# Performance work log

Measured on AMD Instinct MI355X. Metric: run time of the kernel, lower is better.

## Reference

```python
import jax, jax.numpy as jnp
import numpy as np

B = 4          # number of prefill sequences (uniform cu_seqlens)
S = 1024       # tokens per sequence; total_tokens = B*S
SCALE = 0.08838834764831845  # head_dim ** -0.5


def setup_inputs() -> dict:
    key = jax.random.key(0)
    k1, k2, k3 = jax.random.split(key, 3)
    N, H, Hk, D = B * S, 16, 4, 128
    q = jax.random.normal(k1, (N, H, D), dtype=jnp.float32)
    k = jax.random.normal(k2, (N, Hk, D), dtype=jnp.float32)
    v = jax.random.normal(k3, (N, Hk, D), dtype=jnp.float32)
    k_cache = jnp.zeros((N, Hk * D), dtype=jnp.float32)
    v_cache = jnp.zeros((N, Hk * D), dtype=jnp.float32)
    slot_mapping = jnp.arange(N, dtype=jnp.int32)
    return {"q": q, "k": k, "v": v, "k_cache": k_cache,
            "v_cache": v_cache, "slot_mapping": slot_mapping}


def _store_kvcache(k, v, k_cache, v_cache, slot_mapping):
    # scatter token KV into flat paged cache; slot == -1 means skip
    N = k.shape[0]
    valid = slot_mapping >= 0
    slot = jnp.where(valid, slot_mapping, 0)
    k_flat = k.reshape(N, -1)
    v_flat = v.reshape(N, -1)
    kc = k_cache.at[slot].set(jnp.where(valid[:, None], k_flat, k_cache[slot]))
    vc = v_cache.at[slot].set(jnp.where(valid[:, None], v_flat, v_cache[slot]))
    return kc, vc


def _varlen_causal_attn(q, k, v):
    # q: [N, H, D], k/v: [N, Hk, D] with N = B*S uniform sequences (GQA)
    N, H, D = q.shape
    Hk = k.shape[1]
    G = H // Hk
    qb = q.reshape(B, S, Hk, G, D)
    kb = k.reshape(B, S, Hk, D)
    vb = v.reshape(B, S, Hk, D)
    # scores: [B, Hk, G, Sq, Sk]
    scores = jnp.einsum("bqhgd,bkhd->bhgqk", qb, kb) * jnp.float32(SCALE)
    causal = jnp.tril(jnp.ones((S, S), dtype=bool))  # [Sq, Sk]
    scores = jnp.where(causal, scores, jnp.float32(-1e30))
    p = jax.nn.softmax(scores, axis=-1)
    o = jnp.einsum("bhgqk,bkhd->bqhgd", p, vb)
    return o.reshape(N, H, D)


def reference(q, k, v, k_cache, v_cache, slot_mapping):
    kc, vc = _store_kvcache(k, v, k_cache, v_cache, slot_mapping)
    o = _varlen_causal_attn(q, k, v)
    return o, kc, vc
```

## Files before the change

kernel.cpp:

```cpp
#include <hip/hip_runtime.h>

typedef short bf16x8 __attribute__((ext_vector_type(8)));
typedef short bf16x4 __attribute__((ext_vector_type(4)));
typedef float f32x4 __attribute__((ext_vector_type(4)));

#define NB 4
#define SS 1024
#define NH 16
#define NHK 4
#define DD 128
#define NT 16
#define QSCALE 0.08838834764831845f
#define LOG2E 1.4426950408889634f

__device__ __forceinline__ float exp2v(float x) { return __builtin_amdgcn_exp2f(x); }

__device__ __forceinline__ short f2bf(float f) {
  unsigned u = __builtin_bit_cast(unsigned, f);
  u += 0x7fffu + ((u >> 16) & 1u);
  return (short)(u >> 16);
}
__device__ __forceinline__ unsigned pk2(float lo, float hi) {
  return ((unsigned)(unsigned short)f2bf(hi) << 16) | (unsigned)(unsigned short)f2bf(lo);
}

typedef __attribute__((address_space(1))) const unsigned gu32;
typedef __attribute__((address_space(3))) unsigned lu32;
__device__ __forceinline__ void gload16(const void* g, void* l) {
  __builtin_amdgcn_global_load_lds((gu32*)g, (lu32*)l, 16, 0, 0);
}

#define DRAIN_DMA()                                    \
  do {                                                 \
    asm volatile("s_waitcnt vmcnt(0)" ::: "memory");   \
    __builtin_amdgcn_sched_barrier(0);                 \
  } while (0)

__global__ __launch_bounds__(256) void scatter_kv_kernel(
    const float* __restrict__ k, const float* __restrict__ v,
    const int* __restrict__ slot, float* __restrict__ ko, float* __restrict__ vo) {
  int gid = blockIdx.x * blockDim.x + threadIdx.x;
  int tok = gid >> 7;
  int j = gid & 127;
  int s = slot[tok];
  if (s < 0) return;
  ((float4*)(ko + (size_t)s * 512))[j] = ((const float4*)(k + (size_t)tok * 512))[j];
  ((float4*)(vo + (size_t)s * 512))[j] = ((const float4*)(v + (size_t)tok * 512))[j];
}

__global__ __launch_bounds__(256) void prep_kernel(
    const float* __restrict__ k, const float* __restrict__ v,
    const int* __restrict__ slot,
    short* __restrict__ kimg, short* __restrict__ vimg,
    float* __restrict__ ko, float* __restrict__ vo) {
  __shared__ float lvf[64 * 129];
  const int blk = blockIdx.x;
  const int t = blk & 15;
  const int hk = (blk >> 4) & 3;
  const int b = blk >> 6;
  const long tb = (long)b * SS + t * 64;
  const int tid = threadIdx.x;
  short* ki = kimg + (size_t)blk * 8192;
  short* vi = vimg + (size_t)blk * 8192;

#pragma unroll
  for (int p = 0; p < 4; ++p) {
    int c = p * 256 + tid;
    int byte0 = c * 16;
    int row = byte0 >> 8;
    int d0 = (byte0 & 255) >> 1;
    const float* src = k + ((tb + row) * NHK + hk) * DD + d0;
    float4 x = *(const float4*)src;
    float4 y = *(const float4*)(src + 4);
    uint4 pk = {pk2(x.x, x.y), pk2(x.z, x.w), pk2(y.x, y.y), pk2(y.z, y.w)};
    *(uint4*)((char*)ki + (byte0 ^ ((row & 7) << 4))) = pk;
    const float* vs = v + ((tb + row) * NHK + hk) * DD + d0;
    float4 vx = *(const float4*)vs;
    float4 vy = *(const float4*)(vs + 4);
    int sl = slot[tb + row];
    if (sl >= 0) {
      float* kd = ko + (size_t)sl * 512 + hk * 128 + d0;
      *(float4*)kd = x; *(float4*)(kd + 4) = y;
      float* vd = vo + (size_t)sl * 512 + hk * 128 + d0;
      *(float4*)vd = vx; *(float4*)(vd + 4) = vy;
    }
    float* dst = &lvf[row * 129 + d0];
    dst[0] = vx.x; dst[1] = vx.y; dst[2] = vx.z; dst[3] = vx.w;
    dst[4] = vy.x; dst[5] = vy.y; dst[6] = vy.z; dst[7] = vy.w;
  }
  __syncthreads();
#pragma unroll
  for (int p = 0; p < 4; ++p) {
    int c16 = p * 256 + tid;
    int d = c16 >> 3;
    int c8 = c16 & 7;
    int pos0 = c8 * 8;
    int cblk = pos0 >> 5;
    int lg = (pos0 >> 3) & 3;
    int kvb = cblk * 32 + lg * 4;
    float f[8];
#pragma unroll
    for (int j = 0; j < 4; ++j) f[j] = lvf[(kvb + j) * 129 + d];
#pragma unroll
    for (int j = 0; j < 4; ++j) f[4 + j] = lvf[(kvb + 16 + j) * 129 + d];
    uint4 pk = {pk2(f[0], f[1]), pk2(f[2], f[3]), pk2(f[4], f[5]), pk2(f[6], f[7])};
    int byte0 = (d << 7) + (c8 << 4);
    *(uint4*)((char*)vi + (byte0 ^ ((d & 7) << 4))) = pk;
  }
}

__global__ __launch_bounds__(512, 4) void attn_kernel(
    const float* __restrict__ q, const short* __restrict__ kimg,
    const short* __restrict__ vimg, float* __restrict__ o) {
  __shared__ __align__(16) short lk[2][64 * 128];
  __shared__ __align__(16) short lv[2][64 * 128];

  const int tid = threadIdx.x;
  const int l = tid & 63;
  const int w = tid >> 6;
  const int lg = l >> 4;
  const int lr = l & 15;

  const int bid = blockIdx.x;
  const int x = bid & 7;
  const int s_ = bid >> 3;
  const int half = s_ >> 5;
  const int i = s_ & 31;
  const int g16 = x + (half << 3);
  const int hk = g16 & 3;
  const int b = g16 >> 2;
  const int h = hk * 4 + (i >> 3);
  const int jj0 = i & 7;
  const int jj = half ? jj0 : 7 - jj0;

  const int qbase = jj << 7;
  const int tlast = 2 * jj + 1;

  const int q_seq = qbase + w * 16 + lr;
  const long qtok = (long)b * SS + q_seq;

  bf16x8 qf[4];
  {
    const float sc = QSCALE * LOG2E;
    const float* qrow = q + (qtok * NH + h) * DD;
#pragma unroll
    for (int c = 0; c < 4; ++c) {
      int d0 = c * 32 + lg * 8;
      float4 a = *(const float4*)(qrow + d0);
      float4 bb = *(const float4*)(qrow + d0 + 4);
      bf16x8 t;
      t[0] = f2bf(a.x * sc); t[1] = f2bf(a.y * sc);
      t[2] = f2bf(a.z * sc); t[3] = f2bf(a.w * sc);
      t[4] = f2bf(bb.x * sc); t[5] = f2bf(bb.y * sc);
      t[6] = f2bf(bb.z * sc); t[7] = f2bf(bb.w * sc);
      qf[c] = t;
    }
  }

  f32x4 oacc[8];
#pragma unroll
  for (int i2 = 0; i2 < 8; ++i2) oacc[i2] = f32x4{0.f, 0.f, 0.f, 0.f};
  float lsum = 0.f;

  const char* kbase = (const char*)(kimg + ((size_t)g16 * NT) * 8192);
  const char* vbase = (const char*)(vimg + ((size_t)g16 * NT) * 8192);

#define STAGE(buf, tt)                                                \
  {                                                                   \
    const char* ks_ = kbase + (size_t)(tt) * 16384;                   \
    const char* vs_ = vbase + (size_t)(tt) * 16384;                   \
    _Pragma("unroll") for (int p4 = 0; p4 < 2; ++p4) {                \
      int off = p4 * 8192 + tid * 16;                                 \
      gload16(ks_ + off, (char*)lk + (buf) * 16384 + off);            \
      gload16(vs_ + off, (char*)lv + (buf) * 16384 + off);            \
    }                                                                 \
  }

  STAGE(0, 0);
  DRAIN_DMA();
  __syncthreads();

  for (int t = 0; t <= tlast; ++t) {
    const int cur = t & 1;
    if (t < tlast) STAGE(cur ^ 1, t + 1);

    const char* lkc = (const char*)lk[cur];
    const char* lvc = (const char*)lv[cur];

    f32x4 s[4];
#pragma unroll
    for (int kt = 0; kt < 4; ++kt) {
      int row = kt * 16 + lr;
      int rb = row << 8;
      int sw = (row & 7) << 4;
      bf16x8 kf0 = *(const bf16x8*)(lkc + rb + ((0 << 6 | lg << 4) ^ sw));
      bf16x8 kf1 = *(const bf16x8*)(lkc + rb + ((1 << 6 | lg << 4) ^ sw));
      bf16x8 kf2 = *(const bf16x8*)(lkc + rb + ((2 << 6 | lg << 4) ^ sw));
      bf16x8 kf3 = *(const bf16x8*)(lkc + rb + ((3 << 6 | lg << 4) ^ sw));
      f32x4 acc = f32x4{0.f, 0.f, 0.f, 0.f};
      acc = __builtin_amdgcn_mfma_f32_16x16x32_bf16(kf0, qf[0], acc, 0, 0, 0);
      acc = __builtin_amdgcn_mfma_f32_16x16x32_bf16(kf1, qf[1], acc, 0, 0, 0);
      acc = __builtin_amdgcn_mfma_f32_16x16x32_bf16(kf2, qf[2], acc, 0, 0, 0);
      acc = __builtin_amdgcn_mfma_f32_16x16x32_bf16(kf3, qf[3], acc, 0, 0, 0);
      s[kt] = acc;
    }

    if ((t << 6) + 63 > qbase + (w << 4)) {
#pragma unroll
      for (int kt = 0; kt < 4; ++kt)
#pragma unroll
        for (int r = 0; r < 4; ++r) {
          int kvg = (t << 6) + kt * 16 + lg * 4 + r;
          if (kvg > q_seq) s[kt][r] = -1e30f;
        }
    }

    {
      float acc = 0.f;
#pragma unroll
      for (int kt = 0; kt < 4; ++kt)
#pragma unroll
        for (int r = 0; r < 4; ++r) {
          float pp = exp2v(s[kt][r]);
          s[kt][r] = pp;
          acc += pp;
        }
      lsum += acc;
    }

#pragma unroll
    for (int c = 0; c < 2; ++c) {
      unsigned w0, w1, w2, w3;
      asm("v_cvt_pk_bf16_f32 %0, %1, %2" : "=v"(w0) : "v"(s[2 * c][0]), "v"(s[2 * c][1]));
      asm("v_cvt_pk_bf16_f32 %0, %1, %2" : "=v"(w1) : "v"(s[2 * c][2]), "v"(s[2 * c][3]));
      asm("v_cvt_pk_bf16_f32 %0, %1, %2" : "=v"(w2) : "v"(s[2 * c + 1][0]), "v"(s[2 * c + 1][1]));
      asm("v_cvt_pk_bf16_f32 %0, %1, %2" : "=v"(w3) : "v"(s[2 * c + 1][2]), "v"(s[2 * c + 1][3]));
      union { uint4 u; bf16x8 v8; } pu;
      pu.u = uint4{w0, w1, w2, w3};
      bf16x8 pa = pu.v8;
#pragma unroll
      for (int dt = 0; dt < 8; ++dt) {
        int d = dt * 16 + lr;
        int byte = (d << 7) + (((c << 6) | (lg << 4)) ^ ((d & 7) << 4));
        bf16x8 vf = *(const bf16x8*)(lvc + byte);
        oacc[dt] = __builtin_amdgcn_mfma_f32_16x16x32_bf16(pa, vf, oacc[dt], 0, 0, 0);
      }
    }

    DRAIN_DMA();
    __syncthreads();
  }
#undef STAGE

  lsum += __shfl_xor(lsum, 16);
  lsum += __shfl_xor(lsum, 32);
#pragma unroll
  for (int r = 0; r < 4; ++r) {
    float inv = 1.f / __shfl(lsum, (lg << 2) + r);
    long tok = (long)b * SS + qbase + w * 16 + lg * 4 + r;
    float* dst = o + (tok * NH + h) * DD + lr;
#pragma unroll
    for (int dt = 0; dt < 8; ++dt) dst[dt * 16] = oacc[dt][r] * inv;
  }
}

__global__ __launch_bounds__(256) void attn_fallback(
    const float* __restrict__ q, const float* __restrict__ k,
    const float* __restrict__ v, float* __restrict__ o) {
  __shared__ short lk[64 * 128];
  __shared__ short lvt[128 * 64];
  const int tid = threadIdx.x;
  const int l = tid & 63;
  const int w = tid >> 6;
  const int lg = l >> 4;
  const int lr = l & 15;
  const int bid = blockIdx.x;
  const int qt = bid & 15;
  const int h = (bid >> 4) & 15;
  const int b = bid >> 8;
  const int hk = h >> 2;
  const int q_seq = qt * 64 + w * 16 + lr;
  const long qtok = (long)b * SS + q_seq;
  bf16x8 qf[4];
  {
    const float* qrow = q + (qtok * NH + h) * DD;
#pragma unroll
    for (int c = 0; c < 4; ++c) {
      int d0 = c * 32 + lg * 8;
      float4 a = *(const float4*)(qrow + d0);
      float4 bb = *(const float4*)(qrow + d0 + 4);
      bf16x8 t;
      t[0] = f2bf(a.x * QSCALE); t[1] = f2bf(a.y * QSCALE);
      t[2] = f2bf(a.z * QSCALE); t[3] = f2bf(a.w * QSCALE);
      t[4] = f2bf(bb.x * QSCALE); t[5] = f2bf(bb.y * QSCALE);
      t[6] = f2bf(bb.z * QSCALE); t[7] = f2bf(bb.w * QSCALE);
      qf[c] = t;
    }
  }
  f32x4 oacc[8];
#pragma unroll
  for (int i = 0; i < 8; ++i) oacc[i] = f32x4{0.f, 0.f, 0.f, 0.f};
  float m_run = -1e30f, l_run = 0.f;
  const int ntiles = qt + 1;
  for (int t = 0; t < ntiles; ++t) {
    const long tb = (long)b * SS + t * 64;
#pragma unroll
    for (int it = 0; it < 8; ++it) {
      int task = it * 256 + tid;
      int row = task >> 5;
      int dq = (task & 31) << 2;
      float4 xx = *(const float4*)(k + ((tb + row) * NHK + hk) * DD + dq);
      int byte = (row << 8) + (dq << 1);
      byte ^= (row & 7) << 4;
      *(uint2*)((char*)lk + byte) = make_uint2(pk2(xx.x, xx.y), pk2(xx.z, xx.w));
    }
    {
      int a = tid >> 3;
      int e = tid & 7;
      const float* v0r = v + ((tb + 2 * a) * NHK + hk) * DD;
      const float* v1r = v0r + NHK * DD;
#pragma unroll
      for (int i = 0; i < 4; ++i) {
        int d0 = e * 4 + i * 32;
        float4 x0 = *(const float4*)(v0r + d0);
        float4 x1 = *(const float4*)(v1r + d0);
        unsigned pw[4] = {pk2(x0.x, x1.x), pk2(x0.y, x1.y), pk2(x0.z, x1.z), pk2(x0.w, x1.w)};
#pragma unroll
        for (int j = 0; j < 4; ++j) {
          int row = d0 + j;
          int byte = (row << 7) + (a << 2);
          byte ^= (row & 7) << 4;
          *(unsigned*)((char*)lvt + byte) = pw[j];
        }
      }
    }
    __syncthreads();
    f32x4 s[4];
#pragma unroll
    for (int kt = 0; kt < 4; ++kt) {
      f32x4 acc = f32x4{0.f, 0.f, 0.f, 0.f};
      int row = kt * 16 + lr;
#pragma unroll
      for (int c = 0; c < 4; ++c) {
        int byte = (row << 8) + (c << 6) + (lg << 4);
        byte ^= (row & 7) << 4;
        bf16x8 kf = *(const bf16x8*)((const char*)lk + byte);
        acc = __builtin_amdgcn_mfma_f32_16x16x32_bf16(kf, qf[c], acc, 0, 0, 0);
      }
      s[kt] = acc;
    }
    if (t == qt) {
#pragma unroll
      for (int kt = 0; kt < 4; ++kt)
#pragma unroll
        for (int r = 0; r < 4; ++r) {
          int kvg = t * 64 + kt * 16 + lg * 4 + r;
          if (kvg > q_seq) s[kt][r] = -1e30f;
        }
    }
    float mx = -1e30f;
#pragma unroll
    for (int kt = 0; kt < 4; ++kt)
#pragma unroll
      for (int r = 0; r < 4; ++r) mx = fmaxf(mx, s[kt][r]);
    mx = fmaxf(mx, __shfl_xor(mx, 16));
    mx = fmaxf(mx, __shfl_xor(mx, 32));
    float mnew = fmaxf(m_run, mx);
    float resc = expf(m_run - mnew);
    float rsum = 0.f;
#pragma unroll
    for (int kt = 0; kt < 4; ++kt)
#pragma unroll
      for (int r = 0; r < 4; ++r) {
        float pp = expf(s[kt][r] - mnew);
        s[kt][r] = pp;
        rsum += pp;
      }
    rsum += __shfl_xor(rsum, 16);
    rsum += __shfl_xor(rsum, 32);
    l_run = l_run * resc + rsum;
    m_run = mnew;
#pragma unroll
    for (int r = 0; r < 4; ++r) {
      float fr = __shfl(resc, (lg << 2) + r);
#pragma unroll
      for (int dt = 0; dt < 8; ++dt) oacc[dt][r] *= fr;
    }
#pragma unroll
    for (int c = 0; c < 2; ++c) {
      bf16x8 pa;
#pragma unroll
      for (int r = 0; r < 4; ++r) {
        pa[r] = f2bf(s[2 * c][r]);
        pa[r + 4] = f2bf(s[2 * c + 1][r]);
      }
#pragma unroll
      for (int dt = 0; dt < 8; ++dt) {
        int d = dt * 16 + lr;
        int rowbase = d << 7;
        int sw = (d & 7) << 4;
        int b0 = rowbase + (((c << 6) + (lg << 3)) ^ sw);
        int b1 = rowbase + (((c << 6) + 32 + (lg << 3)) ^ sw);
        bf16x4 lo = *(const bf16x4*)((const char*)lvt + b0);
        bf16x4 hi = *(const bf16x4*)((const char*)lvt + b1);
        bf16x8 vf = __builtin_shufflevector(lo, hi, 0, 1, 2, 3, 4, 5, 6, 7);
        oacc[dt] = __builtin_amdgcn_mfma_f32_16x16x32_bf16(pa, vf, oacc[dt], 0, 0, 0);
      }
    }
    __syncthreads();
  }
#pragma unroll
  for (int r = 0; r < 4; ++r) {
    float inv = 1.f / __shfl(l_run, (lg << 2) + r);
    long tok = (long)b * SS + qt * 64 + w * 16 + lg * 4 + r;
    float* dst = o + (tok * NH + h) * DD + lr;
#pragma unroll
    for (int dt = 0; dt < 8; ++dt) dst[dt * 16] = oacc[dt][r] * inv;
  }
}

extern "C" void kernel_launch(void* const* d_in, const int* in_sizes, int n_in,
                              void* d_out, int out_size, void* d_ws, size_t ws_size,
                              hipStream_t stream) {
  const float* q = (const float*)d_in[0];
  const float* k = (const float*)d_in[1];
  const float* v = (const float*)d_in[2];
  const int* slot = (const int*)d_in[5];

  float* out = (float*)d_out;
  float* o_out = out;
  float* k_out = out + (size_t)NB * SS * NH * DD;
  float* v_out = k_out + (size_t)NB * SS * NHK * DD;

  const size_t img_elems = (size_t)NB * NHK * NT * 8192;
  const size_t ws_need = img_elems * 2 * sizeof(short);

  if (ws_size >= ws_need) {
    short* kimg = (short*)d_ws;
    short* vimg = kimg + img_elems;
    prep_kernel<<<NB * NHK * NT, 256, 0, stream>>>(k, v, slot, kimg, vimg, k_out, v_out);
    attn_kernel<<<NB * NH * 8, 512, 0, stream>>>(q, kimg, vimg, o_out);
  } else {
    attn_fallback<<<NB * NH * (SS / 64), 256, 0, stream>>>(q, k, v, o_out);
    scatter_kv_kernel<<<(NB * SS * 128) / 256, 256, 0, stream>>>(k, v, slot, k_out, v_out);
  }
}
```

Before: 46.90 us.

## Switch attention to 32x32x16 MFMA with 4 waves of 32 query rows

Rewrites the attention kernel to use 32x32x16 bf16 MFMA tiles, with each of four waves owning 32 query rows instead of eight waves owning 16. The K and V image layouts and swizzles in the prep kernel change to match the new fragment layout. The P fragments are rearranged in registers with permlane32 swaps instead of going through shared memory. The aim is to get more MFMA work per shared-memory fragment load and to issue fewer instructions, at the cost of higher register pressure and half as many waves per block.

```diff
diff --git a/kernel.cpp b/kernel.cpp
--- a/kernel.cpp
+++ b/kernel.cpp
@@ -3,6 +3,7 @@
 typedef short bf16x8 __attribute__((ext_vector_type(8)));
 typedef short bf16x4 __attribute__((ext_vector_type(4)));
 typedef float f32x4 __attribute__((ext_vector_type(4)));
+typedef float f32x16 __attribute__((ext_vector_type(16)));
 
 #define NB 4
 #define SS 1024
@@ -73,7 +74,7 @@
     float4 x = *(const float4*)src;
     float4 y = *(const float4*)(src + 4);
     uint4 pk = {pk2(x.x, x.y), pk2(x.z, x.w), pk2(y.x, y.y), pk2(y.z, y.w)};
-    *(uint4*)((char*)ki + (byte0 ^ ((row & 7) << 4))) = pk;
+    *(uint4*)((char*)ki + (byte0 ^ ((row & 15) << 4))) = pk;
     const float* vs = v + ((tb + row) * NHK + hk) * DD + d0;
     float4 vx = *(const float4*)vs;
     float4 vy = *(const float4*)(vs + 4);
@@ -93,23 +94,17 @@
   for (int p = 0; p < 4; ++p) {
     int c16 = p * 256 + tid;
     int d = c16 >> 3;
-    int c8 = c16 & 7;
-    int pos0 = c8 * 8;
-    int cblk = pos0 >> 5;
-    int lg = (pos0 >> 3) & 3;
-    int kvb = cblk * 32 + lg * 4;
+    int kv0 = (c16 & 7) << 3;
     float f[8];
 #pragma unroll
-    for (int j = 0; j < 4; ++j) f[j] = lvf[(kvb + j) * 129 + d];
-#pragma unroll
-    for (int j = 0; j < 4; ++j) f[4 + j] = lvf[(kvb + 16 + j) * 129 + d];
+    for (int j = 0; j < 8; ++j) f[j] = lvf[(kv0 + j) * 129 + d];
     uint4 pk = {pk2(f[0], f[1]), pk2(f[2], f[3]), pk2(f[4], f[5]), pk2(f[6], f[7])};
-    int byte0 = (d << 7) + (c8 << 4);
-    *(uint4*)((char*)vi + (byte0 ^ ((d & 7) << 4))) = pk;
-  }
-}
-
-__global__ __launch_bounds__(512, 4) void attn_kernel(
+    int dest = (d << 7) + ((kv0 << 1) ^ ((d & 7) << 4));
+    *(uint4*)((char*)vi + dest) = pk;
+  }
+}
+
+__global__ __launch_bounds__(256, 2) void attn_kernel(
     const float* __restrict__ q, const short* __restrict__ kimg,
     const short* __restrict__ vimg, float* __restrict__ o) {
   __shared__ __align__(16) short lk[2][64 * 128];
@@ -118,8 +113,8 @@
   const int tid = threadIdx.x;
   const int l = tid & 63;
   const int w = tid >> 6;
-  const int lg = l >> 4;
-  const int lr = l & 15;
+  const int hi = l >> 5;
+  const int lq = l & 31;
 
   const int bid = blockIdx.x;
   const int x = bid & 7;
@@ -136,30 +131,33 @@
   const int qbase = jj << 7;
   const int tlast = 2 * jj + 1;
 
-  const int q_seq = qbase + w * 16 + lr;
+  const int q_seq = qbase + (w << 5) + lq;
   const long qtok = (long)b * SS + q_seq;
 
-  bf16x8 qf[4];
+  bf16x8 qf[8];
   {
     const float sc = QSCALE * LOG2E;
     const float* qrow = q + (qtok * NH + h) * DD;
 #pragma unroll
-    for (int c = 0; c < 4; ++c) {
-      int d0 = c * 32 + lg * 8;
+    for (int ks = 0; ks < 8; ++ks) {
+      int d0 = ks * 16 + hi * 8;
       float4 a = *(const float4*)(qrow + d0);
       float4 bb = *(const float4*)(qrow + d0 + 4);
-      bf16x8 t;
-      t[0] = f2bf(a.x * sc); t[1] = f2bf(a.y * sc);
-      t[2] = f2bf(a.z * sc); t[3] = f2bf(a.w * sc);
-      t[4] = f2bf(bb.x * sc); t[5] = f2bf(bb.y * sc);
-      t[6] = f2bf(bb.z * sc); t[7] = f2bf(bb.w * sc);
-      qf[c] = t;
-    }
-  }
-
-  f32x4 oacc[8];
-#pragma unroll
-  for (int i2 = 0; i2 < 8; ++i2) oacc[i2] = f32x4{0.f, 0.f, 0.f, 0.f};
+      bf16x8 tt;
+      tt[0] = f2bf(a.x * sc); tt[1] = f2bf(a.y * sc);
+      tt[2] = f2bf(a.z * sc); tt[3] = f2bf(a.w * sc);
+      tt[4] = f2bf(bb.x * sc); tt[5] = f2bf(bb.y * sc);
+      tt[6] = f2bf(bb.z * sc); tt[7] = f2bf(bb.w * sc);
+      qf[ks] = tt;
+    }
+  }
+
+  f32x16 zeroes;
+#pragma unroll
+  for (int r = 0; r < 16; ++r) zeroes[r] = 0.f;
+  f32x16 oacc[4];
+#pragma unroll
+  for (int d = 0; d < 4; ++d) oacc[d] = zeroes;
   float lsum = 0.f;
 
   const char* kbase = (const char*)(kimg + ((size_t)g16 * NT) * 8192);
@@ -169,8 +167,8 @@
   {                                                                   \
     const char* ks_ = kbase + (size_t)(tt) * 16384;                   \
     const char* vs_ = vbase + (size_t)(tt) * 16384;                   \
-    _Pragma("unroll") for (int p4 = 0; p4 < 2; ++p4) {                \
-      int off = p4 * 8192 + tid * 16;                                 \
+    _Pragma("unroll") for (int p4 = 0; p4 < 4; ++p4) {                \
+      int off = p4 * 4096 + tid * 16;                                 \
       gload16(ks_ + off, (char*)lk + (buf) * 16384 + off);            \
       gload16(vs_ + off, (char*)lv + (buf) * 16384 + off);            \
     }                                                                 \
@@ -187,63 +185,68 @@
     const char* lkc = (const char*)lk[cur];
     const char* lvc = (const char*)lv[cur];
 
-    f32x4 s[4];
-#pragma unroll
-    for (int kt = 0; kt < 4; ++kt) {
-      int row = kt * 16 + lr;
-      int rb = row << 8;
-      int sw = (row & 7) << 4;
-      bf16x8 kf0 = *(const bf16x8*)(lkc + rb + ((0 << 6 | lg << 4) ^ sw));
-      bf16x8 kf1 = *(const bf16x8*)(lkc + rb + ((1 << 6 | lg << 4) ^ sw));
-      bf16x8 kf2 = *(const bf16x8*)(lkc + rb + ((2 << 6 | lg << 4) ^ sw));
-      bf16x8 kf3 = *(const bf16x8*)(lkc + rb + ((3 << 6 | lg << 4) ^ sw));
-      f32x4 acc = f32x4{0.f, 0.f, 0.f, 0.f};
-      acc = __builtin_amdgcn_mfma_f32_16x16x32_bf16(kf0, qf[0], acc, 0, 0, 0);
-      acc = __builtin_amdgcn_mfma_f32_16x16x32_bf16(kf1, qf[1], acc, 0, 0, 0);
-      acc = __builtin_amdgcn_mfma_f32_16x16x32_bf16(kf2, qf[2], acc, 0, 0, 0);
-      acc = __builtin_amdgcn_mfma_f32_16x16x32_bf16(kf3, qf[3], acc, 0, 0, 0);
-      s[kt] = acc;
-    }
-
-    if ((t << 6) + 63 > qbase + (w << 4)) {
-#pragma unroll
-      for (int kt = 0; kt < 4; ++kt)
-#pragma unroll
-        for (int r = 0; r < 4; ++r) {
-          int kvg = (t << 6) + kt * 16 + lg * 4 + r;
-          if (kvg > q_seq) s[kt][r] = -1e30f;
-        }
+    f32x16 s0 = zeroes, s1 = zeroes;
+    {
+      const int rb0 = lq << 8;
+      const int rb1 = (32 + lq) << 8;
+      const int sw = (lq & 15) << 4;
+#pragma unroll
+      for (int ks = 0; ks < 8; ++ks) {
+        int off = ((ks << 5) + (hi << 4)) ^ sw;
+        bf16x8 kf0 = *(const bf16x8*)(lkc + rb0 + off);
+        bf16x8 kf1 = *(const bf16x8*)(lkc + rb1 + off);
+        s0 = __builtin_amdgcn_mfma_f32_32x32x16_bf16(kf0, qf[ks], s0, 0, 0, 0);
+        s1 = __builtin_amdgcn_mfma_f32_32x32x16_bf16(kf1, qf[ks], s1, 0, 0, 0);
+      }
+    }
+
+    if ((t << 6) + 63 > qbase + (w << 5)) {
+#pragma unroll
+      for (int r = 0; r < 16; ++r) {
+        int kvr = (t << 6) + (r & 3) + ((r >> 2) << 3) + (hi << 2);
+        if (kvr > q_seq) s0[r] = -1e30f;
+        if (kvr + 32 > q_seq) s1[r] = -1e30f;
+      }
     }
 
     {
       float acc = 0.f;
 #pragma unroll
-      for (int kt = 0; kt < 4; ++kt)
-#pragma unroll
-        for (int r = 0; r < 4; ++r) {
-          float pp = exp2v(s[kt][r]);
-          s[kt][r] = pp;
-          acc += pp;
-        }
+      for (int r = 0; r < 16; ++r) {
+        float p0 = exp2v(s0[r]); s0[r] = p0;
+        float p1 = exp2v(s1[r]); s1[r] = p1;
+        acc += p0 + p1;
+      }
       lsum += acc;
     }
 
-#pragma unroll
-    for (int c = 0; c < 2; ++c) {
-      unsigned w0, w1, w2, w3;
-      asm("v_cvt_pk_bf16_f32 %0, %1, %2" : "=v"(w0) : "v"(s[2 * c][0]), "v"(s[2 * c][1]));
-      asm("v_cvt_pk_bf16_f32 %0, %1, %2" : "=v"(w1) : "v"(s[2 * c][2]), "v"(s[2 * c][3]));
-      asm("v_cvt_pk_bf16_f32 %0, %1, %2" : "=v"(w2) : "v"(s[2 * c + 1][0]), "v"(s[2 * c + 1][1]));
-      asm("v_cvt_pk_bf16_f32 %0, %1, %2" : "=v"(w3) : "v"(s[2 * c + 1][2]), "v"(s[2 * c + 1][3]));
-      union { uint4 u; bf16x8 v8; } pu;
-      pu.u = uint4{w0, w1, w2, w3};
-      bf16x8 pa = pu.v8;
-#pragma unroll
-      for (int dt = 0; dt < 8; ++dt) {
-        int d = dt * 16 + lr;
-        int byte = (d << 7) + (((c << 6) | (lg << 4)) ^ ((d & 7) << 4));
-        bf16x8 vf = *(const bf16x8*)(lvc + byte);
-        oacc[dt] = __builtin_amdgcn_mfma_f32_16x16x32_bf16(pa, vf, oacc[dt], 0, 0, 0);
+    bf16x8 pa[4];
+#pragma unroll
+    for (int sub = 0; sub < 2; ++sub) {
+#pragma unroll
+      for (int m = 0; m < 2; ++m) {
+        f32x16 P = sub ? s1 : s0;
+        unsigned A, B, C, D;
+        asm("v_cvt_pk_bf16_f32 %0, %1, %2" : "=v"(A) : "v"(P[8 * m + 0]), "v"(P[8 * m + 1]));
+        asm("v_cvt_pk_bf16_f32 %0, %1, %2" : "=v"(B) : "v"(P[8 * m + 2]), "v"(P[8 * m + 3]));
+        asm("v_cvt_pk_bf16_f32 %0, %1, %2" : "=v"(C) : "v"(P[8 * m + 4]), "v"(P[8 * m + 5]));
+        asm("v_cvt_pk_bf16_f32 %0, %1, %2" : "=v"(D) : "v"(P[8 * m + 6]), "v"(P[8 * m + 7]));
+        asm("v_permlane32_swap_b32 %0, %1" : "+v"(A), "+v"(C));
+        asm("v_permlane32_swap_b32 %0, %1" : "+v"(B), "+v"(D));
+        union { uint4 u; bf16x8 v8; } pu;
+        pu.u = uint4{A, B, C, D};
+        pa[sub * 2 + m] = pu.v8;
+      }
+    }
+
+#pragma unroll
+    for (int ds = 0; ds < 4; ++ds) {
+      const int rb = ((ds << 5) + lq) << 7;
+      const int sw = (lq & 7) << 4;
+#pragma unroll
+      for (int m = 0; m < 4; ++m) {
+        bf16x8 vf = *(const bf16x8*)(lvc + rb + (((m << 5) + (hi << 4)) ^ sw));
+        oacc[ds] = __builtin_amdgcn_mfma_f32_32x32x16_bf16(pa[m], vf, oacc[ds], 0, 0, 0);
       }
     }
 
@@ -252,15 +255,17 @@
   }
 #undef STAGE
 
-  lsum += __shfl_xor(lsum, 16);
   lsum += __shfl_xor(lsum, 32);
 #pragma unroll
-  for (int r = 0; r < 4; ++r) {
-    float inv = 1.f / __shfl(lsum, (lg << 2) + r);
-    long tok = (long)b * SS + qbase + w * 16 + lg * 4 + r;
-    float* dst = o + (tok * NH + h) * DD + lr;
-#pragma unroll
-    for (int dt = 0; dt < 8; ++dt) dst[dt * 16] = oacc[dt][r] * inv;
+  for (int r = 0; r < 16; ++r) {
+    int qloc = (r & 3) + ((r >> 2) << 3) + (hi << 2);
+    float inv = 1.f / __shfl(lsum, qloc);
+    long tok = (long)b * SS + qbase + (w << 5) + qloc;
+    float* dst = o + (tok * NH + h) * DD + lq;
+    dst[0]  = oacc[0][r] * inv;
+    dst[32] = oacc[1][r] * inv;
+    dst[64] = oacc[2][r] * inv;
+    dst[96] = oacc[3][r] * inv;
   }
 }
 
@@ -402,8 +407,8 @@
         int b0 = rowbase + (((c << 6) + (lg << 3)) ^ sw);
         int b1 = rowbase + (((c << 6) + 32 + (lg << 3)) ^ sw);
         bf16x4 lo = *(const bf16x4*)((const char*)lvt + b0);
-        bf16x4 hi = *(const bf16x4*)((const char*)lvt + b1);
-        bf16x8 vf = __builtin_shufflevector(lo, hi, 0, 1, 2, 3, 4, 5, 6, 7);
+        bf16x4 hi2 = *(const bf16x4*)((const char*)lvt + b1);
+        bf16x8 vf = __builtin_shufflevector(lo, hi2, 0, 1, 2, 3, 4, 5, 6, 7);
         oacc[dt] = __builtin_amdgcn_mfma_f32_16x16x32_bf16(pa, vf, oacc[dt], 0, 0, 0);
       }
     }
@@ -439,7 +444,7 @@
     short* kimg = (short*)d_ws;
     short* vimg = kimg + img_elems;
     prep_kernel<<<NB * NHK * NT, 256, 0, stream>>>(k, v, slot, kimg, vimg, k_out, v_out);
-    attn_kernel<<<NB * NH * 8, 512, 0, stream>>>(q, kimg, vimg, o_out);
+    attn_kernel<<<NB * NH * 8, 256, 0, stream>>>(q, kimg, vimg, o_out);
   } else {
     attn_fallback<<<NB * NH * (SS / 64), 256, 0, stream>>>(q, k, v, o_out);
     scatter_kv_kernel<<<(NB * SS * 128) / 256, 256, 0, stream>>>(k, v, slot, k_out, v_out);
```

Measured after the change: 48.06 us. 1.02x slower.
